# Performance work log

Hardware: AMD Instinct MI355X
Metric: run time of the kernel (lower is better)

## Reference

```python
import jax, jax.numpy as jnp
import numpy as np

B, N, D, P, H = 16, 1024, 512, 512, 8
E = P // H  # head dim = 64


def layer_norm(x, g, b, eps=1e-5):
    mu = jnp.mean(x, axis=-1, keepdims=True)
    var = jnp.var(x, axis=-1, keepdims=True)
    return (x - mu) * jax.lax.rsqrt(var + eps) * g + b


def setup_inputs() -> dict:
    key = jax.random.key(0)
    ks = jax.random.split(key, 12)
    s = 0.02
    inp = {
        "x": jax.random.normal(ks[0], (B, N, D), dtype=jnp.float32),
        "Wq": jax.random.normal(ks[1], (D, P), dtype=jnp.float32) * s,
        "bq": jnp.zeros((P,), jnp.float32),
        "Wk": jax.random.normal(ks[2], (D, P), dtype=jnp.float32) * s,
        "bk": jnp.zeros((P,), jnp.float32),
        "Wv": jax.random.normal(ks[3], (D, P), dtype=jnp.float32) * s,
        "bv": jnp.zeros((P,), jnp.float32),
        "Wo": jax.random.normal(ks[4], (P, D), dtype=jnp.float32) * s,
        "bo": jnp.zeros((D,), jnp.float32),
        "ln1_g": jnp.ones((D,), jnp.float32),
        "ln1_b": jnp.zeros((D,), jnp.float32),
        "W1": jax.random.normal(ks[5], (D, 4 * D), dtype=jnp.float32) * s,
        "b1": jnp.zeros((4 * D,), jnp.float32),
        "W2": jax.random.normal(ks[6], (4 * D, D), dtype=jnp.float32) * s,
        "b2": jnp.zeros((D,), jnp.float32),
        "ln2_g": jnp.ones((D,), jnp.float32),
        "ln2_b": jnp.zeros((D,), jnp.float32),
    }
    return inp


def reference(x, Wq, bq, Wk, bk, Wv, bv, Wo, bo, ln1_g, ln1_b, W1, b1, W2, b2, ln2_g, ln2_b):
    # dropout layers are identity in eval mode
    q = (x @ Wq + bq).reshape(B, N, H, E)
    k = (x @ Wk + bk).reshape(B, N, H, E)
    v = (x @ Wv + bv).reshape(B, N, H, E)
    scale = 1.0 / jnp.sqrt(jnp.float32(E))
    scores = jnp.einsum('blhe,bshe->bhls', q, k)  # [B,H,L,S]
    A = jax.nn.softmax(scale * scores, axis=-1)
    V = jnp.einsum('bhls,bshd->blhd', A, v).reshape(B, N, P)
    att = V @ Wo + bo
    x1 = layer_norm(x + att, ln1_g, ln1_b)
    # FFN: 1x1 convs over channel dim == per-token linears, exact GELU
    ff = jax.nn.gelu(x1 @ W1 + b1, approximate=False) @ W2 + b2
    return layer_norm(x1 + ff, ln2_g, ln2_b)
```

## Files before the change

### kernel.cpp

```cpp
#include <hip/hip_runtime.h>
#include <hip/hip_bf16.h>

typedef __hip_bfloat16 bf16;
typedef __bf16 bf16x8 __attribute__((ext_vector_type(8)));
typedef __bf16 bf16x4 __attribute__((ext_vector_type(4)));
typedef float f32x4 __attribute__((ext_vector_type(4)));
typedef float f32x16 __attribute__((ext_vector_type(16)));
typedef unsigned u32x4 __attribute__((ext_vector_type(4)));

static __device__ __forceinline__ f32x4 mfma16(bf16x8 a, bf16x8 b, f32x4 c) {
  return __builtin_amdgcn_mfma_f32_16x16x32_bf16(a, b, c, 0, 0, 0);
}
static __device__ __forceinline__ f32x16 mfma32(bf16x8 a, bf16x8 b, f32x16 c) {
  return __builtin_amdgcn_mfma_f32_32x32x16_bf16(a, b, c, 0, 0, 0);
}
static __device__ __forceinline__ bf16x8 ld8(const bf16* p) {
  return *reinterpret_cast<const bf16x8*>(p);
}
static __device__ __forceinline__ float toF(float v) { return v; }
static __device__ __forceinline__ float toF(bf16 v) { return __bfloat162float(v); }
static __device__ __forceinline__ void stF(float* p, float v) { *p = v; }
static __device__ __forceinline__ void stF(bf16* p, float v) { *p = __float2bfloat16(v); }
static __device__ __forceinline__ unsigned pk2(float lo, float hi) {
  unsigned a = __bfloat16_as_ushort(__float2bfloat16(lo));
  unsigned b = __bfloat16_as_ushort(__float2bfloat16(hi));
  return (b << 16) | a;
}

typedef __attribute__((address_space(1))) void gvoid;
typedef __attribute__((address_space(3))) void lvoid;
static __device__ __forceinline__ void gl2lds16(const bf16* g, bf16* l) {
  __builtin_amdgcn_global_load_lds((gvoid*)g, (lvoid*)l, 16, 0, 0);
}

__global__ __launch_bounds__(256) void cvt_kernel(const float* __restrict__ in,
                                                  bf16* __restrict__ out) {
  long i = (long)blockIdx.x * 256 + threadIdx.x;
  float4 v = reinterpret_cast<const float4*>(in)[i];
  bf16x4 o;
  o[0] = __float2bfloat16(v.x); o[1] = __float2bfloat16(v.y);
  o[2] = __float2bfloat16(v.z); o[3] = __float2bfloat16(v.w);
  reinterpret_cast<bf16x4*>(out)[i] = o;
}

__global__ void prep_weights(const float* __restrict__ Wq, const float* __restrict__ Wk,
                             const float* __restrict__ Wv, const float* __restrict__ Wo,
                             const float* __restrict__ W1, const float* __restrict__ W2,
                             bf16* __restrict__ Wtqkv, bf16* __restrict__ WtO,
                             bf16* __restrict__ Wt1, bf16* __restrict__ Wt2) {
  int id = blockIdx.x;
  const float* in;
  bf16* out;
  int K, N, n0, k0;
  if (id < 1024) {
    int which = id >> 8, t = id & 255;
    K = 512; N = 512;
    n0 = (t & 15) * 32; k0 = (t >> 4) * 32;
    if (which == 0)      { in = Wq; out = Wtqkv; }
    else if (which == 1) { in = Wk; out = Wtqkv + (size_t)512 * 512; }
    else if (which == 2) { in = Wv; out = Wtqkv + (size_t)1024 * 512; }
    else                 { in = Wo; out = WtO; }
  } else if (id < 2048) {
    int t = id - 1024;
    in = W1; out = Wt1; K = 512; N = 2048;
    n0 = (t & 63) * 32; k0 = (t >> 6) * 32;
  } else {
    int t = id - 2048;
    in = W2; out = Wt2; K = 2048; N = 512;
    n0 = (t & 15) * 32; k0 = (t >> 4) * 32;
  }
  __shared__ float tile[32][33];
  int tx = threadIdx.x, ty = threadIdx.y;
#pragma unroll
  for (int j = 0; j < 32; j += 8)
    tile[ty + j][tx] = in[(long)(k0 + ty + j) * N + n0 + tx];
  __syncthreads();
#pragma unroll
  for (int j = 0; j < 32; j += 8)
    out[(long)(n0 + ty + j) * K + k0 + tx] = __float2bfloat16(tile[tx][ty + j]);
}

template <int MODE>
__global__ __launch_bounds__(256) void gemm_kernel(
    const bf16* __restrict__ A, const bf16* __restrict__ Wt,
    const float* __restrict__ b0, const float* __restrict__ b1_,
    const float* __restrict__ b2_, bf16* C0, bf16* C1, bf16* C2,
    int K, int ldc, int mmask, int mshift) {
  __shared__ alignas(16) bf16 As[2][128 * 32];
  __shared__ alignas(16) bf16 Bs[2][128 * 32];
  const int tid = threadIdx.x;
  const int wave = tid >> 6, lane = tid & 63;
  const int lr = lane & 15, lq = lane >> 4;
  const int L = blockIdx.x;
  const int m0 = (L & mmask) * 128, n0 = (L >> mshift) * 128;
  const int wm = (wave >> 1) * 64, wn = (wave & 1) * 64;

  const int srow0 = (wave * 2) * 16 + (lane >> 2);
  const int srow1 = (wave * 2 + 1) * 16 + (lane >> 2);
  const int scol = (lane & 3) * 8;
  const bf16* Ag0 = A + (long)(m0 + srow0) * K + scol;
  const bf16* Ag1 = A + (long)(m0 + srow1) * K + scol;
  const bf16* Bg0 = Wt + (long)(n0 + srow0) * K + scol;
  const bf16* Bg1 = Wt + (long)(n0 + srow1) * K + scol;
  const int so0 = (wave * 2) * 16 * 32;
  const int so1 = (wave * 2 + 1) * 16 * 32;

  f32x4 acc[4][4] = {};

  gl2lds16(Ag0, &As[0][so0]);
  gl2lds16(Ag1, &As[0][so1]);
  gl2lds16(Bg0, &Bs[0][so0]);
  gl2lds16(Bg1, &Bs[0][so1]);
  __syncthreads();

  int p = 0;
  for (int k0 = 0; k0 < K; k0 += 32) {
    int kn = k0 + 32;
    if (kn < K) {
      gl2lds16(Ag0 + kn, &As[p ^ 1][so0]);
      gl2lds16(Ag1 + kn, &As[p ^ 1][so1]);
      gl2lds16(Bg0 + kn, &Bs[p ^ 1][so0]);
      gl2lds16(Bg1 + kn, &Bs[p ^ 1][so1]);
    }
    bf16x8 af[4], bfr[4];
#pragma unroll
    for (int i = 0; i < 4; ++i) af[i] = ld8(&As[p][(wm + i * 16 + lr) * 32 + lq * 8]);
#pragma unroll
    for (int j = 0; j < 4; ++j) bfr[j] = ld8(&Bs[p][(wn + j * 16 + lr) * 32 + lq * 8]);
#pragma unroll
    for (int i = 0; i < 4; ++i)
#pragma unroll
      for (int j = 0; j < 4; ++j) acc[i][j] = mfma16(af[i], bfr[j], acc[i][j]);
    __syncthreads();
    p ^= 1;
  }

  const float* bias = b0;
  bf16* C = C0;
  int cb = n0;
  bool vmode = false;
  if (MODE == 2) {
    if (n0 >= 1024)     { bias = b2_; C = C2; cb = n0 - 1024; vmode = true; }
    else if (n0 >= 512) { bias = b1_; C = C1; cb = n0 - 512; }
  }

#pragma unroll
  for (int i = 0; i < 4; ++i) {
#pragma unroll
    for (int j = 0; j < 4; ++j) {
      int col = cb + wn + j * 16 + lr;
      float bv = bias[col];
#pragma unroll
      for (int rr = 0; rr < 4; ++rr) {
        int row = m0 + wm + i * 16 + lq * 4 + rr;
        float v = acc[i][j][rr] + bv;
        if (MODE == 1) v = 0.5f * v * (1.0f + erff(v * 0.70710678118654752f));
        if (MODE == 2 && vmode) {
          int hh = col >> 6, e = col & 63;
          int bb = row >> 10, tok = row & 1023;
          C[(((long)((bb * 8 + hh) * 64 + e)) << 10) + tok] = __float2bfloat16(v);
        } else {
          C[(long)row * ldc + col] = __float2bfloat16(v);
        }
      }
    }
  }
}

__global__ __launch_bounds__(256, 4) void attn32(
    const bf16* __restrict__ Q, const bf16* __restrict__ Km,
    const bf16* __restrict__ Vt, bf16* __restrict__ O) {
  __shared__ alignas(16) float lred[4][32];
  const int tid = threadIdx.x;
  const int wave = tid >> 6, lane = tid & 63;
  const int l31 = lane & 31, lh = lane >> 5;
  const int bi = blockIdx.x;
  const int bh = bi & 127;
  const int qt = (bi >> 7) * 4 + wave;
  const int h = bh & 7, b = bh >> 3;
  const int q0 = qt * 32;
  const float Cc = 0.18033688011112042f;

  bf16x8 qf[4];
  const bf16* qp = Q + (long)(b * 1024 + q0 + l31) * 512 + h * 64 + lh * 8;
#pragma unroll
  for (int et = 0; et < 4; ++et) qf[et] = ld8(qp + et * 16);

  const bf16* kpt = Km + (long)(b * 1024 + l31) * 512 + h * 64 + lh * 8;
  const bf16* vp0 = Vt + ((long)((b * 8 + h) * 64 + l31)) * 1024 + lh * 8;
  const bf16* vp1 = vp0 + (long)32 * 1024;

  f32x16 oacc[2] = {};
  float lsum = 0.f;

  for (int t = 0; t < 32; ++t) {
    bf16x8 kf[4], vf0a, vf0b, vf1a, vf1b;
#pragma unroll
    for (int et = 0; et < 4; ++et) kf[et] = ld8(kpt + et * 16);
    vf0a = ld8(vp0);
    vf0b = ld8(vp0 + 16);
    vf1a = ld8(vp1);
    vf1b = ld8(vp1 + 16);

    f32x16 s = {};
#pragma unroll
    for (int et = 0; et < 4; ++et) s = mfma32(kf[et], qf[et], s);

    float pr[16];
#pragma unroll
    for (int r = 0; r < 16; ++r) { pr[r] = exp2f(s[r] * Cc); lsum += pr[r]; }

    unsigned w0 = pk2(pr[0], pr[1]),   w1 = pk2(pr[2], pr[3]);
    unsigned w2 = pk2(pr[4], pr[5]),   w3 = pk2(pr[6], pr[7]);
    unsigned w4 = pk2(pr[8], pr[9]),   w5 = pk2(pr[10], pr[11]);
    unsigned w6 = pk2(pr[12], pr[13]), w7 = pk2(pr[14], pr[15]);
    auto r02 = __builtin_amdgcn_permlane32_swap(w0, w2, false, false);
    auto r13 = __builtin_amdgcn_permlane32_swap(w1, w3, false, false);
    auto r46 = __builtin_amdgcn_permlane32_swap(w4, w6, false, false);
    auto r57 = __builtin_amdgcn_permlane32_swap(w5, w7, false, false);
    u32x4 a0 = {r02[0], r13[0], r02[1], r13[1]};
    u32x4 a1 = {r46[0], r57[0], r46[1], r57[1]};
    bf16x8 pf0 = __builtin_bit_cast(bf16x8, a0);
    bf16x8 pf1 = __builtin_bit_cast(bf16x8, a1);

    oacc[0] = mfma32(pf0, vf0a, oacc[0]);
    oacc[1] = mfma32(pf0, vf1a, oacc[1]);
    oacc[0] = mfma32(pf1, vf0b, oacc[0]);
    oacc[1] = mfma32(pf1, vf1b, oacc[1]);

    kpt += 32 * 512;
    vp0 += 32;
    vp1 += 32;
  }

  lsum += __shfl_xor(lsum, 32);
  if (lh == 0) lred[wave][l31] = lsum;
  __syncthreads();

  float linv[16];
#pragma unroll
  for (int g = 0; g < 4; ++g) {
    f32x4 lvv = *(const f32x4*)&lred[wave][g * 8 + 4 * lh];
#pragma unroll
    for (int j = 0; j < 4; ++j) linv[g * 4 + j] = 1.f / lvv[j];
  }

  const long rowbase = (long)(b * 1024 + q0);
#pragma unroll
  for (int et = 0; et < 2; ++et) {
    bf16* obase = O + rowbase * 512 + h * 64 + et * 32 + l31;
#pragma unroll
    for (int r = 0; r < 16; ++r) {
      int q = (r & 3) + 8 * (r >> 2) + 4 * lh;
      obase[(long)q * 512] = __float2bfloat16(oacc[et][r] * linv[r]);
    }
  }
}

template <typename TX, typename TO>
__global__ __launch_bounds__(256) void add_ln_kernel(
    const TX* __restrict__ X, const bf16* __restrict__ Y,
    const float* __restrict__ g, const float* __restrict__ bb,
    TO* __restrict__ out) {
  const int row = blockIdx.x, t = threadIdx.x;
  __shared__ float s1[4], s2[4];
  long base = (long)row * 512;
  float v0 = toF(X[base + t]) + toF(Y[base + t]);
  float v1 = toF(X[base + 256 + t]) + toF(Y[base + 256 + t]);
  float s = v0 + v1, q = v0 * v0 + v1 * v1;
#pragma unroll
  for (int o = 32; o > 0; o >>= 1) {
    s += __shfl_down(s, o);
    q += __shfl_down(q, o);
  }
  int wv = t >> 6;
  if ((t & 63) == 0) { s1[wv] = s; s2[wv] = q; }
  __syncthreads();
  float St = s1[0] + s1[1] + s1[2] + s1[3];
  float Qt = s2[0] + s2[1] + s2[2] + s2[3];
  float mean = St * (1.f / 512.f);
  float var = Qt * (1.f / 512.f) - mean * mean;
  float rs = rsqrtf(var + 1e-5f);
  stF(&out[base + t], (v0 - mean) * rs * g[t] + bb[t]);
  stF(&out[base + 256 + t], (v1 - mean) * rs * g[256 + t] + bb[256 + t]);
}

extern "C" void kernel_launch(void* const* d_in, const int* in_sizes, int n_in,
                              void* d_out, int out_size, void* d_ws, size_t ws_size,
                              hipStream_t stream) {
  const float* x    = (const float*)d_in[0];
  const float* Wq   = (const float*)d_in[1];
  const float* bq   = (const float*)d_in[2];
  const float* Wk   = (const float*)d_in[3];
  const float* bk   = (const float*)d_in[4];
  const float* Wv   = (const float*)d_in[5];
  const float* bv   = (const float*)d_in[6];
  const float* Wo   = (const float*)d_in[7];
  const float* bo   = (const float*)d_in[8];
  const float* ln1g = (const float*)d_in[9];
  const float* ln1b = (const float*)d_in[10];
  const float* W1   = (const float*)d_in[11];
  const float* b1   = (const float*)d_in[12];
  const float* W2   = (const float*)d_in[13];
  const float* b2   = (const float*)d_in[14];
  const float* ln2g = (const float*)d_in[15];
  const float* ln2b = (const float*)d_in[16];
  float* out = (float*)d_out;

  char* ws = (char*)d_ws;
  size_t off = 0;
  auto alloc = [&](size_t bytes) {
    char* p = ws + off;
    off += (bytes + 255) & ~(size_t)255;
    return (bf16*)p;
  };
  bf16* Wtqkv = alloc((size_t)1536 * 512 * 2);
  bf16* WtO   = alloc((size_t)512 * 512 * 2);
  bf16* Wt1   = alloc((size_t)512 * 2048 * 2);
  bf16* Wt2   = alloc((size_t)2048 * 512 * 2);
  const size_t SB = (size_t)16384 * 512 * 2;

  dim3 tb(32, 8);

  if (ws_size >= (size_t)104 * 1024 * 1024) {
    bf16* xb  = alloc(SB);
    bf16* kb  = alloc(SB);
    bf16* qb  = alloc(SB);
    bf16* vtb = alloc(SB);
    bf16* p0  = alloc(SB);
    bf16* p1  = alloc(SB);
    bf16* ff1 = qb;
    bf16* ff2 = xb;
    (void)p0; (void)p1;

    cvt_kernel<<<8192, 256, 0, stream>>>(x, xb);
    prep_weights<<<3072, tb, 0, stream>>>(Wq, Wk, Wv, Wo, W1, W2,
                                          Wtqkv, WtO, Wt1, Wt2);
    gemm_kernel<2><<<1536, 256, 0, stream>>>(xb, Wtqkv, bq, bk, bv,
                                             qb, kb, vtb, 512, 512, 127, 7);
    attn32<<<1024, 256, 0, stream>>>(qb, kb, vtb, qb);
    gemm_kernel<0><<<512, 256, 0, stream>>>(qb, WtO, bo, nullptr, nullptr,
                                            vtb, nullptr, nullptr, 512, 512, 127, 7);
    add_ln_kernel<bf16, bf16><<<16384, 256, 0, stream>>>(xb, vtb, ln1g, ln1b, kb);
    gemm_kernel<1><<<2048, 256, 0, stream>>>(kb, Wt1, b1, nullptr, nullptr,
                                             ff1, nullptr, nullptr, 512, 2048, 127, 7);
    gemm_kernel<0><<<512, 256, 0, stream>>>(ff1, Wt2, b2, nullptr, nullptr,
                                            ff2, nullptr, nullptr, 2048, 512, 127, 7);
    add_ln_kernel<bf16, float><<<16384, 256, 0, stream>>>(kb, ff2, ln2g, ln2b, out);
  } else {
    bf16* xb  = alloc(SB);
    bf16* kb  = alloc(SB);
    bf16* qb  = alloc(SB);
    bf16* vtb = alloc(SB);
    bf16* fb  = alloc(SB / 2);
    bf16* ff1 = qb;

    cvt_kernel<<<8192, 256, 0, stream>>>(x, xb);
    prep_weights<<<3072, tb, 0, stream>>>(Wq, Wk, Wv, Wo, W1, W2,
                                          Wtqkv, WtO, Wt1, Wt2);
    gemm_kernel<2><<<1536, 256, 0, stream>>>(xb, Wtqkv, bq, bk, bv,
                                             qb, kb, vtb, 512, 512, 127, 7);
    attn32<<<1024, 256, 0, stream>>>(qb, kb, vtb, qb);
    gemm_kernel<0><<<512, 256, 0, stream>>>(qb, WtO, bo, nullptr, nullptr,
                                            vtb, nullptr, nullptr, 512, 512, 127, 7);
    add_ln_kernel<bf16, bf16><<<16384, 256, 0, stream>>>(xb, vtb, ln1g, ln1b, kb);

    for (int hh = 0; hh < 2; ++hh) {
      const bf16* x1h = kb + (size_t)hh * 8192 * 512;
      gemm_kernel<1><<<1024, 256, 0, stream>>>(x1h, Wt1, b1, nullptr, nullptr,
                                               ff1, nullptr, nullptr, 512, 2048, 63, 6);
      gemm_kernel<0><<<256, 256, 0, stream>>>(ff1, Wt2, b2, nullptr, nullptr,
                                              fb, nullptr, nullptr, 2048, 512, 63, 6);
      add_ln_kernel<bf16, float><<<8192, 256, 0, stream>>>(x1h, fb, ln2g, ln2b,
                                                           out + (size_t)hh * 8192 * 512);
    }
  }
}
```

Measured before the change: 438.5 us.

## Stage K/V tiles in double-buffered shared memory for attention kernel

```diff
diff --git a/kernel.cpp b/kernel.cpp
--- a/kernel.cpp
+++ b/kernel.cpp
@@ -170,6 +170,8 @@
 __global__ __launch_bounds__(256, 4) void attn32(
     const bf16* __restrict__ Q, const bf16* __restrict__ Km,
     const bf16* __restrict__ Vt, bf16* __restrict__ O) {
+  __shared__ alignas(16) bf16 Ks[2][32][68];
+  __shared__ alignas(16) bf16 Vs[2][64][36];
   __shared__ alignas(16) float lred[4][32];
   const int tid = threadIdx.x;
   const int wave = tid >> 6, lane = tid & 63;
@@ -181,39 +183,50 @@
   const int q0 = qt * 32;
   const float Cc = 0.18033688011112042f;
 
+  const int kr = tid >> 3, kc = tid & 7;
+  const int vr = tid >> 2, vc = tid & 3;
+  const bf16* Kg = Km + (long)(b * 1024 + kr) * 512 + h * 64 + kc * 8;
+  const bf16* Vg = Vt + (long)((b * 8 + h) * 64 + vr) * 1024 + vc * 8;
+
   bf16x8 qf[4];
   const bf16* qp = Q + (long)(b * 1024 + q0 + l31) * 512 + h * 64 + lh * 8;
 #pragma unroll
   for (int et = 0; et < 4; ++et) qf[et] = ld8(qp + et * 16);
 
-  const bf16* kpt = Km + (long)(b * 1024 + l31) * 512 + h * 64 + lh * 8;
-  const bf16* vp0 = Vt + ((long)((b * 8 + h) * 64 + l31)) * 1024 + lh * 8;
-  const bf16* vp1 = vp0 + (long)32 * 1024;
+  bf16x8 rK = ld8(Kg), rV = ld8(Vg);
+  *reinterpret_cast<bf16x8*>(&Ks[0][kr][kc * 8]) = rK;
+  *reinterpret_cast<bf16x8*>(&Vs[0][vr][vc * 8]) = rV;
+  rK = ld8(Kg + (long)32 * 512);
+  rV = ld8(Vg + 32);
+  __syncthreads();
 
   f32x16 oacc[2] = {};
   float lsum = 0.f;
 
+#pragma unroll 1
   for (int t = 0; t < 32; ++t) {
-    bf16x8 kf[4], vf0a, vf0b, vf1a, vf1b;
-#pragma unroll
-    for (int et = 0; et < 4; ++et) kf[et] = ld8(kpt + et * 16);
-    vf0a = ld8(vp0);
-    vf0b = ld8(vp0 + 16);
-    vf1a = ld8(vp1);
-    vf1b = ld8(vp1 + 16);
+    const int buf = t & 1;
+    bf16x8 kf[4];
+#pragma unroll
+    for (int et = 0; et < 4; ++et)
+      kf[et] = ld8(&Ks[buf][l31][lh * 8 + et * 16]);
 
     f32x16 s = {};
 #pragma unroll
     for (int et = 0; et < 4; ++et) s = mfma32(kf[et], qf[et], s);
 
-    float pr[16];
-#pragma unroll
-    for (int r = 0; r < 16; ++r) { pr[r] = exp2f(s[r] * Cc); lsum += pr[r]; }
-
-    unsigned w0 = pk2(pr[0], pr[1]),   w1 = pk2(pr[2], pr[3]);
-    unsigned w2 = pk2(pr[4], pr[5]),   w3 = pk2(pr[6], pr[7]);
-    unsigned w4 = pk2(pr[8], pr[9]),   w5 = pk2(pr[10], pr[11]);
-    unsigned w6 = pk2(pr[12], pr[13]), w7 = pk2(pr[14], pr[15]);
+    bf16x8 vf0 = ld8(&Vs[buf][l31][lh * 8]);
+    bf16x8 vf1 = ld8(&Vs[buf][l31][16 + lh * 8]);
+    bf16x8 vf2 = ld8(&Vs[buf][32 + l31][lh * 8]);
+    bf16x8 vf3 = ld8(&Vs[buf][32 + l31][16 + lh * 8]);
+
+#pragma unroll
+    for (int r = 0; r < 16; ++r) { s[r] = exp2f(s[r] * Cc); lsum += s[r]; }
+
+    unsigned w0 = pk2(s[0], s[1]),   w1 = pk2(s[2], s[3]);
+    unsigned w2 = pk2(s[4], s[5]),   w3 = pk2(s[6], s[7]);
+    unsigned w4 = pk2(s[8], s[9]),   w5 = pk2(s[10], s[11]);
+    unsigned w6 = pk2(s[12], s[13]), w7 = pk2(s[14], s[15]);
     auto r02 = __builtin_amdgcn_permlane32_swap(w0, w2, false, false);
     auto r13 = __builtin_amdgcn_permlane32_swap(w1, w3, false, false);
     auto r46 = __builtin_amdgcn_permlane32_swap(w4, w6, false, false);
@@ -223,14 +236,20 @@
     bf16x8 pf0 = __builtin_bit_cast(bf16x8, a0);
     bf16x8 pf1 = __builtin_bit_cast(bf16x8, a1);
 
-    oacc[0] = mfma32(pf0, vf0a, oacc[0]);
-    oacc[1] = mfma32(pf0, vf1a, oacc[1]);
-    oacc[0] = mfma32(pf1, vf0b, oacc[0]);
-    oacc[1] = mfma32(pf1, vf1b, oacc[1]);
-
-    kpt += 32 * 512;
-    vp0 += 32;
-    vp1 += 32;
+    oacc[0] = mfma32(pf0, vf0, oacc[0]);
+    oacc[1] = mfma32(pf0, vf2, oacc[1]);
+    oacc[0] = mfma32(pf1, vf1, oacc[0]);
+    oacc[1] = mfma32(pf1, vf3, oacc[1]);
+
+    if (t < 31) {
+      *reinterpret_cast<bf16x8*>(&Ks[buf ^ 1][kr][kc * 8]) = rK;
+      *reinterpret_cast<bf16x8*>(&Vs[buf ^ 1][vr][vc * 8]) = rV;
+      if (t < 30) {
+        rK = ld8(Kg + (long)(t + 2) * 32 * 512);
+        rV = ld8(Vg + (t + 2) * 32);
+      }
+      __syncthreads();
+    }
   }
 
   lsum += __shfl_xor(lsum, 32);
```

New measurement: 441.2 us. No clear change (+0.6%).
